# Performance work log

Measured on AMD Instinct MI355X. Metric: run time of the kernel, lower is better.

Reference implementation:

```python
import jax, jax.numpy as jnp
import numpy as np
from jax import lax

B, IMG, P, CIN = 8, 224, 16, 3
D, NH, E, HID, DEPTH, NC = 768, 12, 4, 3072, 12, 1000
NPAT = (IMG // P) ** 2  # 196
S = NPAT + 1            # 197 tokens incl cls
HD = D // NH            # 64
EPS = 1e-5


def _ln(x, g, b):
    m = jnp.mean(x, axis=-1, keepdims=True)
    v = jnp.mean((x - m) ** 2, axis=-1, keepdims=True)
    return (x - m) * lax.rsqrt(v + EPS) * g + b


def setup_inputs() -> dict:
    key = jax.random.key(0)
    ks = list(jax.random.split(key, 24))
    def rn(k, shape, s=0.02):
        return (jax.random.normal(k, shape) * s).astype(jnp.float32)
    inp = {
        "x": jax.random.normal(ks[0], (B, CIN, IMG, IMG), dtype=jnp.float32),
        "patch_w": rn(ks[1], (D, CIN, P, P)),
        "patch_b": jnp.zeros((D,), jnp.float32),
        "cls_token": jnp.zeros((1, 1, D), jnp.float32),
        "pos_embed": rn(ks[2], (1, S, D)),
        "ln1_g": jnp.ones((DEPTH, D), jnp.float32),
        "ln1_b": jnp.zeros((DEPTH, D), jnp.float32),
        "ln2_g": jnp.ones((DEPTH, D), jnp.float32),
        "ln2_b": jnp.zeros((DEPTH, D), jnp.float32),
        "attn_in_w": rn(ks[3], (DEPTH, 3 * D, D)),
        "attn_in_b": jnp.zeros((DEPTH, 3 * D), jnp.float32),
        "attn_out_w": rn(ks[4], (DEPTH, D, D)),
        "attn_out_b": jnp.zeros((DEPTH, D), jnp.float32),
        "gate_w": rn(ks[5], (DEPTH, E, D)),
        "gate_b": jnp.zeros((DEPTH, E), jnp.float32),
        "w1": rn(ks[6], (DEPTH, E, D, HID)),
        "b1": jnp.zeros((DEPTH, E, HID), jnp.float32),
        "w2": rn(ks[7], (DEPTH, E, HID, D)),
        "b2": jnp.zeros((DEPTH, E, D), jnp.float32),
        "head_w": rn(ks[8], (NC, D)),
        "head_b": jnp.zeros((NC,), jnp.float32),
    }
    return inp


def _forward(x, patch_w, patch_b, cls_token, pos_embed, ln1_g, ln1_b, ln2_g, ln2_b,
             attn_in_w, attn_in_b, attn_out_w, attn_out_b, gate_w, gate_b,
             w1, b1, w2, b2, head_w, head_b):
    # Patch embedding: conv stride=patch, then flatten spatial -> tokens
    feat = lax.conv_general_dilated(x, patch_w, window_strides=(P, P), padding="VALID",
                                    dimension_numbers=("NCHW", "OIHW", "NCHW"))
    t = feat.reshape(B, D, NPAT).transpose(0, 2, 1) + patch_b  # [B, 196, D]
    cls = jnp.broadcast_to(cls_token, (B, 1, D))
    h = jnp.concatenate([cls, t], axis=1) + pos_embed  # [B, S, D]

    scale = 1.0 / np.sqrt(HD).astype(np.float32)
    for i in range(DEPTH):
        # ---- attention (query = LN(x); key/value = x, as in source) ----
        qn = _ln(h, ln1_g[i], ln1_b[i])
        wq, wk, wv = attn_in_w[i, :D], attn_in_w[i, D:2 * D], attn_in_w[i, 2 * D:]
        bq, bk, bv = attn_in_b[i, :D], attn_in_b[i, D:2 * D], attn_in_b[i, 2 * D:]
        q = (qn @ wq.T + bq).reshape(B, S, NH, HD)
        k = (h @ wk.T + bk).reshape(B, S, NH, HD)
        v = (h @ wv.T + bv).reshape(B, S, NH, HD)
        scores = jnp.einsum("bqhd,bkhd->bhqk", q, k) * scale
        attn = jax.nn.softmax(scores, axis=-1)
        o = jnp.einsum("bhqk,bkhd->bqhd", attn, v).reshape(B, S, D)
        h = h + o @ attn_out_w[i].T + attn_out_b[i]

        # ---- Top-1 gated MoE MLP ----
        y = _ln(h, ln2_g[i], ln2_b[i])
        logits = y @ gate_w[i].T + gate_b[i]            # [B,S,E]
        probs = jax.nn.softmax(logits, axis=-1)
        top = jnp.argmax(probs, axis=-1)                # [B,S]
        onehot = jax.nn.one_hot(top, E, dtype=y.dtype)  # [B,S,E]
        gv = jnp.sum(probs * onehot, axis=-1)           # [B,S] top-1 gate score
        hidd = jax.nn.gelu(jnp.einsum("bsd,edh->besh", y, w1[i]) + b1[i][None, :, None, :])
        eout = jnp.einsum("besh,ehd->besd", hidd, w2[i]) + b2[i][None, :, None, :]
        moe = jnp.einsum("bse,besd->bsd", onehot, eout) * gv[..., None]
        h = h + moe

    return h[:, 0] @ head_w.T + head_b  # [B, NC]


def reference(x, patch_w, patch_b, cls_token, pos_embed, ln1_g, ln1_b, ln2_g, ln2_b,
              attn_in_w, attn_in_b, attn_out_w, attn_out_b, gate_w, gate_b,
              w1, b1, w2, b2, head_w, head_b):
    return _forward(x, patch_w, patch_b, cls_token, pos_embed, ln1_g, ln1_b, ln2_g,
                    ln2_b, attn_in_w, attn_in_b, attn_out_w, attn_out_b, gate_w,
                    gate_b, w1, b1, w2, b2, head_w, head_b)
```

## Files before the change

### kernel.cpp

```cpp
#include <hip/hip_runtime.h>
#include <math.h>


#define BB 8
#define SS 197
#define DD 768
#define MT (BB*SS)
#define NPATCH 196
#define MPE (BB*NPATCH)
#define HHID 3072
#define NEXP 4
#define QKVN 2304
#define SCW 228

typedef __bf16 bf16_t;
typedef bf16_t bf16x4 __attribute__((ext_vector_type(4)));
typedef bf16_t bf16x8 __attribute__((ext_vector_type(8)));
typedef float  f32x4  __attribute__((ext_vector_type(4)));

__device__ __forceinline__ void gload16(const bf16_t* g, bf16_t* l) {
    __builtin_amdgcn_global_load_lds(
        (const __attribute__((address_space(1))) unsigned int*)g,
        (__attribute__((address_space(3))) unsigned int*)l,
        16, 0, 0);
}

__device__ __forceinline__ bf16x8 cvt8(float4 a, float4 b) {
    bf16x8 o;
    o[0]=(bf16_t)a.x; o[1]=(bf16_t)a.y; o[2]=(bf16_t)a.z; o[3]=(bf16_t)a.w;
    o[4]=(bf16_t)b.x; o[5]=(bf16_t)b.y; o[6]=(bf16_t)b.z; o[7]=(bf16_t)b.w;
    return o;
}

__global__ void gather_patches(const float* __restrict__ x, bf16_t* __restrict__ Xp) {
    int i = blockIdx.x * 256 + threadIdx.x;
    if (i >= MPE * DD) return;
    int k = i % DD;
    int m = i / DD;
    int pw = k & 15, ph = (k >> 4) & 15, cin = k >> 8;
    int px = m % 14, py = (m / 14) % 14, b = m / NPATCH;
    int row = py * 16 + ph, col = px * 16 + pw;
    Xp[i] = (bf16_t)x[((size_t)(b * 3 + cin) * 224 + row) * 224 + col];
}

__global__ void build_h(const float* __restrict__ pe, const float* __restrict__ patch_b,
                        const float* __restrict__ cls, const float* __restrict__ pos,
                        float* __restrict__ h, bf16_t* __restrict__ hb) {
    int i = blockIdx.x * 256 + threadIdx.x;
    if (i >= MT * DD) return;
    int d = i % DD;
    int s = (i / DD) % SS;
    int b = i / (DD * SS);
    float v;
    if (s == 0) v = cls[d];
    else        v = pe[((size_t)(b * NPATCH) + (s - 1)) * DD + d] + patch_b[d];
    float vv = v + pos[s * DD + d];
    h[i] = vv;
    hb[i] = (bf16_t)vv;
}

__global__ void cvt_bf16(const float* __restrict__ in, bf16_t* __restrict__ out, int n) {
    int i = (blockIdx.x * 256 + threadIdx.x) * 8;
    if (i >= n) return;
    const float4* p = (const float4*)(in + i);
    *(bf16x8*)(out + i) = cvt8(p[0], p[1]);
}

__global__ __launch_bounds__(256) void transpose_cvt(const float* __restrict__ in,
                                                     bf16_t* __restrict__ out, int R, int C) {
    int z = blockIdx.z;
    in  += (size_t)z * R * C;
    out += (size_t)z * R * C;
    __shared__ float t[32][33];
    int c0 = blockIdx.x * 32, r0 = blockIdx.y * 32;
    int tx = threadIdx.x & 31, ty = threadIdx.x >> 5;
    #pragma unroll
    for (int i = 0; i < 4; i++)
        t[ty + 8*i][tx] = in[(size_t)(r0 + ty + 8*i) * C + c0 + tx];
    __syncthreads();
    #pragma unroll
    for (int i = 0; i < 4; i++)
        out[(size_t)(c0 + ty + 8*i) * R + r0 + tx] = (bf16_t)t[tx][ty + 8*i];
}

template<int BM, int BN, int WM, int WN, int MODE>
__global__ __launch_bounds__((BM/WM)*(BN/WN)*64) void gemm_bf16(
    const bf16_t* __restrict__ A, const bf16_t* __restrict__ A2, int nsplit,
    const bf16_t* __restrict__ Bw,
    const float* __restrict__ bias, float* __restrict__ C, bf16_t* __restrict__ Cb,
    const int* __restrict__ cnt, const int* __restrict__ idx,
    const float* __restrict__ gv, int M, int N, int K)
{
    constexpr int NW  = (BM/WM)*(BN/WN);
    constexpr int WNC = BN/WN;
    constexpr int MI  = WM/16;
    constexpr int NI  = WN/16;
    constexpr int IA  = (BM/8)/NW;
    constexpr int IB  = (BN/8)/NW;
    constexpr bool GATHER = (MODE == 3 || MODE == 4);

    int z = blockIdx.z;
    int count = GATHER ? cnt[z] : M;
    int m0 = blockIdx.y * BM;
    if (m0 >= count) return;
    int n0 = blockIdx.x * BN;
    if (n0 >= nsplit) A = A2;
    Bw += (size_t)z * N * K;
    const float* biasz = bias ? (bias + (size_t)z * N) : nullptr;

    __shared__ bf16_t As[2][BM * 64];
    __shared__ bf16_t Bs[2][BN * 64];
    __shared__ int toks[BM];

    int tid = threadIdx.x, lane = tid & 63, w = tid >> 6;
    if (tid < BM) {
        int mm = m0 + tid;
        if (mm > count - 1) mm = count - 1;
        toks[tid] = GATHER ? idx[z * MT + mm] : mm;
    }
    __syncthreads();

    int wm = (w / WNC) * WM, wn = (w % WNC) * WN;
    int fr = lane & 15, fs = lane >> 4;

    f32x4 acc[MI][NI];
    #pragma unroll
    for (int mi = 0; mi < MI; mi++)
        #pragma unroll
        for (int ni = 0; ni < NI; ni++)
            #pragma unroll
            for (int j = 0; j < 4; j++) acc[mi][ni][j] = 0.f;

    int nk = K >> 6;
    int srow = lane >> 3, scc = lane & 7;

    #define STAGE(buf, k0)                                                              \
        {                                                                               \
            _Pragma("unroll")                                                           \
            for (int i = 0; i < IA; i++) {                                              \
                int blk = i*NW + w;                                                     \
                int row = blk*8 + srow;                                                 \
                const bf16_t* s = A + (size_t)toks[row] * K + (k0) + ((scc ^ (row & 7)) << 3); \
                gload16(s, &As[buf][blk * 512]);                                        \
            }                                                                           \
            _Pragma("unroll")                                                           \
            for (int i = 0; i < IB; i++) {                                              \
                int blk = i*NW + w;                                                     \
                int row = blk*8 + srow;                                                 \
                const bf16_t* s = Bw + (size_t)(n0 + row) * K + (k0) + ((scc ^ (row & 7)) << 3); \
                gload16(s, &Bs[buf][blk * 512]);                                        \
            }                                                                           \
        }

    STAGE(0, 0);
    __syncthreads();
    int cur = 0;
    for (int t = 0; t < nk; t++) {
        if (t + 1 < nk) STAGE(cur ^ 1, (t + 1) << 6);
        #pragma unroll
        for (int ks = 0; ks < 2; ks++) {
            bf16x8 af[MI], bfr[NI];
            #pragma unroll
            for (int mi = 0; mi < MI; mi++) {
                int r = wm + mi * 16 + fr;
                af[mi] = *(bf16x8*)&As[cur][r * 64 + (((fs + ks*4) ^ (r & 7)) << 3)];
            }
            #pragma unroll
            for (int ni = 0; ni < NI; ni++) {
                int r = wn + ni * 16 + fr;
                bfr[ni] = *(bf16x8*)&Bs[cur][r * 64 + (((fs + ks*4) ^ (r & 7)) << 3)];
            }
            #pragma unroll
            for (int mi = 0; mi < MI; mi++)
                #pragma unroll
                for (int ni = 0; ni < NI; ni++)
                    acc[mi][ni] = __builtin_amdgcn_mfma_f32_16x16x32_bf16(af[mi], bfr[ni], acc[mi][ni], 0, 0, 0);
        }
        __syncthreads();
        cur ^= 1;
    }
    #undef STAGE

    #pragma unroll
    for (int mi = 0; mi < MI; mi++) {
        #pragma unroll
        for (int j = 0; j < 4; j++) {
            int rr = wm + mi * 16 + fs * 4 + j;
            if (m0 + rr >= count) continue;
            int crow = toks[rr];
            #pragma unroll
            for (int ni = 0; ni < NI; ni++) {
                int col = n0 + wn + ni * 16 + fr;
                float v = acc[mi][ni][j];
                if (MODE >= 2) v += biasz[col];
                if (MODE == 0) C[(size_t)crow * N + col] = v;
                else if (MODE == 2) C[(size_t)crow * N + col] += v;
                else if (MODE == 3) {
                    float g = 0.5f * v * (1.0f + tanhf(0.7978845608028654f * (v + 0.044715f * v * v * v)));
                    Cb[(size_t)crow * N + col] = (bf16_t)g;
                } else if (MODE == 4) {
                    float* p = &C[(size_t)crow * N + col];
                    float nv = *p + v * gv[crow];
                    *p = nv;
                    Cb[(size_t)crow * N + col] = (bf16_t)nv;
                } else {
                    Cb[(size_t)crow * N + col] = (bf16_t)v;
                }
            }
        }
    }
}

__global__ __launch_bounds__(256) void ln1_kernel(const float* __restrict__ x,
                                                  const float* __restrict__ g,
                                                  const float* __restrict__ b,
                                                  bf16_t* __restrict__ qn)
{
    int wid = (blockIdx.x * 256 + threadIdx.x) >> 6;
    if (wid >= MT) return;
    int lane = threadIdx.x & 63;
    const float4* xr = (const float4*)(x + (size_t)wid * DD);
    float4 v0 = xr[lane], v1 = xr[lane + 64], v2 = xr[lane + 128];
    float s = v0.x+v0.y+v0.z+v0.w + v1.x+v1.y+v1.z+v1.w + v2.x+v2.y+v2.z+v2.w;
    #pragma unroll
    for (int o = 32; o > 0; o >>= 1) s += __shfl_xor(s, o);
    float mean = s * (1.0f/DD);
    float s2 = 0.f;
    #pragma unroll
    for (int c = 0; c < 3; c++) {
        float4 v = c == 0 ? v0 : (c == 1 ? v1 : v2);
        float dx = v.x-mean, dy = v.y-mean, dz = v.z-mean, dw = v.w-mean;
        s2 += dx*dx + dy*dy + dz*dz + dw*dw;
    }
    #pragma unroll
    for (int o = 32; o > 0; o >>= 1) s2 += __shfl_xor(s2, o);
    float rs = rsqrtf(s2 * (1.0f/DD) + 1e-5f);
    const float4* gr = (const float4*)g;
    const float4* br = (const float4*)b;
    #pragma unroll
    for (int c = 0; c < 3; c++) {
        float4 v = c == 0 ? v0 : (c == 1 ? v1 : v2);
        float4 gg = gr[lane + 64*c], bb = br[lane + 64*c];
        bf16x4 o;
        o[0] = (bf16_t)((v.x - mean) * rs * gg.x + bb.x);
        o[1] = (bf16_t)((v.y - mean) * rs * gg.y + bb.y);
        o[2] = (bf16_t)((v.z - mean) * rs * gg.z + bb.z);
        o[3] = (bf16_t)((v.w - mean) * rs * gg.w + bb.w);
        *(bf16x4*)(qn + (size_t)wid * DD + (lane + 64*c) * 4) = o;
    }
}

__global__ __launch_bounds__(256) void ln2_gate_kernel(const float* __restrict__ x,
                                                       const float* __restrict__ g,
                                                       const float* __restrict__ b,
                                                       const float* __restrict__ gw,
                                                       const float* __restrict__ gb,
                                                       bf16_t* __restrict__ yb,
                                                       float* __restrict__ gv,
                                                       int* __restrict__ cnt,
                                                       int* __restrict__ idxb)
{
    int wid = (blockIdx.x * 256 + threadIdx.x) >> 6;
    if (wid >= MT) return;
    int lane = threadIdx.x & 63;
    const float4* xr = (const float4*)(x + (size_t)wid * DD);
    float4 v0 = xr[lane], v1 = xr[lane + 64], v2 = xr[lane + 128];
    float s = v0.x+v0.y+v0.z+v0.w + v1.x+v1.y+v1.z+v1.w + v2.x+v2.y+v2.z+v2.w;
    #pragma unroll
    for (int o = 32; o > 0; o >>= 1) s += __shfl_xor(s, o);
    float mean = s * (1.0f/DD);
    float s2 = 0.f;
    #pragma unroll
    for (int c = 0; c < 3; c++) {
        float4 v = c == 0 ? v0 : (c == 1 ? v1 : v2);
        float dx = v.x-mean, dy = v.y-mean, dz = v.z-mean, dw = v.w-mean;
        s2 += dx*dx + dy*dy + dz*dz + dw*dw;
    }
    #pragma unroll
    for (int o = 32; o > 0; o >>= 1) s2 += __shfl_xor(s2, o);
    float rs = rsqrtf(s2 * (1.0f/DD) + 1e-5f);
    const float4* gr = (const float4*)g;
    const float4* br = (const float4*)b;
    float p0 = 0.f, p1 = 0.f, p2 = 0.f, p3 = 0.f;
    #pragma unroll
    for (int c = 0; c < 3; c++) {
        float4 v = c == 0 ? v0 : (c == 1 ? v1 : v2);
        float4 gg = gr[lane + 64*c], bb = br[lane + 64*c];
        float y0 = (v.x - mean) * rs * gg.x + bb.x;
        float y1 = (v.y - mean) * rs * gg.y + bb.y;
        float y2 = (v.z - mean) * rs * gg.z + bb.z;
        float y3 = (v.w - mean) * rs * gg.w + bb.w;
        bf16x4 o; o[0]=(bf16_t)y0; o[1]=(bf16_t)y1; o[2]=(bf16_t)y2; o[3]=(bf16_t)y3;
        *(bf16x4*)(yb + (size_t)wid * DD + (lane + 64*c) * 4) = o;
        int off = lane + 64*c;
        float4 w0 = ((const float4*)(gw          ))[off];
        float4 w1v = ((const float4*)(gw +   DD  ))[off];
        float4 w2v = ((const float4*)(gw + 2*DD  ))[off];
        float4 w3v = ((const float4*)(gw + 3*DD  ))[off];
        p0 += y0*w0.x + y1*w0.y + y2*w0.z + y3*w0.w;
        p1 += y0*w1v.x + y1*w1v.y + y2*w1v.z + y3*w1v.w;
        p2 += y0*w2v.x + y1*w2v.y + y2*w2v.z + y3*w2v.w;
        p3 += y0*w3v.x + y1*w3v.y + y2*w3v.z + y3*w3v.w;
    }
    #pragma unroll
    for (int o = 32; o > 0; o >>= 1) {
        p0 += __shfl_xor(p0, o); p1 += __shfl_xor(p1, o);
        p2 += __shfl_xor(p2, o); p3 += __shfl_xor(p3, o);
    }
    if (lane == 0) {
        float l0 = p0 + gb[0], l1 = p1 + gb[1], l2 = p2 + gb[2], l3 = p3 + gb[3];
        int top = 0; float best = l0;
        if (l1 > best) { best = l1; top = 1; }
        if (l2 > best) { best = l2; top = 2; }
        if (l3 > best) { best = l3; top = 3; }
        float Z = __expf(l0-best) + __expf(l1-best) + __expf(l2-best) + __expf(l3-best);
        gv[wid] = 1.0f / Z;
        int pos = atomicAdd(&cnt[top], 1);
        idxb[top * MT + pos] = wid;
    }
}

__global__ __launch_bounds__(256) void attn_kernel(const bf16_t* __restrict__ qkv,
                                                   bf16_t* __restrict__ ob)
{
    int qt = blockIdx.x, hh = blockIdx.y, b = blockIdx.z;
    __shared__ bf16_t Qs[64 * 64];
    __shared__ bf16_t KV[64 * 68];
    __shared__ float  Sc[64 * SCW];
    __shared__ float  linv[64];

    int tid = threadIdx.x, lane = tid & 63, w = tid >> 6;
    int wm = (w >> 1) * 32, wn = (w & 1) * 32;
    int fr = lane & 15, fs = lane >> 4;

    #pragma unroll
    for (int it = 0; it < 2; it++) {
        int row = 8*(it*4 + w) + (lane >> 3), cc = lane & 7;
        int q = qt*64 + row; if (q > SS-1) q = SS-1;
        const bf16_t* src = qkv + ((size_t)(b*SS + q))*QKVN + hh*64 + ((cc ^ (row & 7)) << 3);
        gload16(src, &Qs[(it*4 + w) * 512]);
    }

    for (int kt = 0; kt < 4; kt++) {
        __syncthreads();
        #pragma unroll
        for (int it = 0; it < 2; it++) {
            int row = 8*(it*4 + w) + (lane >> 3), cc = lane & 7;
            int k = kt*64 + row; if (k > SS-1) k = SS-1;
            const bf16_t* src = qkv + ((size_t)(b*SS + k))*QKVN + 768 + hh*64 + ((cc ^ (row & 7)) << 3);
            gload16(src, &KV[(it*4 + w) * 512]);
        }
        __syncthreads();
        f32x4 acc[2][2];
        #pragma unroll
        for (int mi = 0; mi < 2; mi++)
            #pragma unroll
            for (int ni = 0; ni < 2; ni++)
                #pragma unroll
                for (int j = 0; j < 4; j++) acc[mi][ni][j] = 0.f;
        #pragma unroll
        for (int ks = 0; ks < 2; ks++) {
            bf16x8 af[2], bfr[2];
            #pragma unroll
            for (int mi = 0; mi < 2; mi++) {
                int r = wm + mi * 16 + fr;
                af[mi] = *(bf16x8*)&Qs[r * 64 + (((fs + ks*4) ^ (r & 7)) << 3)];
            }
            #pragma unroll
            for (int ni = 0; ni < 2; ni++) {
                int r = wn + ni * 16 + fr;
                bfr[ni] = *(bf16x8*)&KV[r * 64 + (((fs + ks*4) ^ (r & 7)) << 3)];
            }
            #pragma unroll
            for (int mi = 0; mi < 2; mi++)
                #pragma unroll
                for (int ni = 0; ni < 2; ni++)
                    acc[mi][ni] = __builtin_amdgcn_mfma_f32_16x16x32_bf16(af[mi], bfr[ni], acc[mi][ni], 0, 0, 0);
        }
        #pragma unroll
        for (int mi = 0; mi < 2; mi++)
            #pragma unroll
            for (int j = 0; j < 4; j++) {
                int qr = wm + mi * 16 + fs * 4 + j;
                #pragma unroll
                for (int ni = 0; ni < 2; ni++) {
                    int col = kt*64 + wn + ni * 16 + fr;
                    if (col < SCW) {
                        float v = acc[mi][ni][j] * 0.125f;
                        if (col > SS-1) v = -1e30f;
                        Sc[qr * SCW + col] = v;
                    }
                }
            }
    }
    __syncthreads();

    {
        int row = tid >> 2, c = tid & 3;
        float m = -1e30f;
        for (int i = c; i < SCW; i += 4) m = fmaxf(m, Sc[row * SCW + i]);
        m = fmaxf(m, __shfl_xor(m, 1, 4));
        m = fmaxf(m, __shfl_xor(m, 2, 4));
        float s = 0.f;
        for (int i = c; i < SCW; i += 4) {
            float e = __expf(Sc[row * SCW + i] - m);
            Sc[row * SCW + i] = e;
            s += e;
        }
        s += __shfl_xor(s, 1, 4);
        s += __shfl_xor(s, 2, 4);
        if (c == 0) linv[row] = 1.0f / s;
    }

    f32x4 pv[2][2];
    #pragma unroll
    for (int mi = 0; mi < 2; mi++)
        #pragma unroll
        for (int ni = 0; ni < 2; ni++)
            #pragma unroll
            for (int j = 0; j < 4; j++) pv[mi][ni][j] = 0.f;

    for (int kt = 0; kt < 4; kt++) {
        __syncthreads();
        {
            int s = tid >> 2, c2 = tid & 3;
            int k = kt*64 + s; if (k > SS-1) k = SS-1;
            const bf16_t* vr = qkv + ((size_t)(b*SS + k))*QKVN + 1536 + hh*64;
            bf16x8 v0 = *(const bf16x8*)(vr + c2*16);
            bf16x8 v1 = *(const bf16x8*)(vr + c2*16 + 8);
            #pragma unroll
            for (int j = 0; j < 8; j++) {
                KV[(c2*16 + j) * 68 + s]     = v0[j];
                KV[(c2*16 + 8 + j) * 68 + s] = v1[j];
            }
        }
        __syncthreads();
        #pragma unroll
        for (int ks = 0; ks < 2; ks++) {
            int s0 = kt*64 + ks*32;
            if (s0 > SS-1) continue;
            bf16x8 af[2], bfr[2];
            #pragma unroll
            for (int mi = 0; mi < 2; mi++) {
                int qr = wm + mi * 16 + fr;
                const float* p = &Sc[qr * SCW + s0 + fs * 8];
                af[mi] = cvt8(*(const float4*)p, *(const float4*)(p + 4));
            }
            #pragma unroll
            for (int ni = 0; ni < 2; ni++) {
                int d = wn + ni * 16 + fr;
                bfr[ni] = *(bf16x8*)&KV[d * 68 + ks*32 + fs*8];
            }
            #pragma unroll
            for (int mi = 0; mi < 2; mi++)
                #pragma unroll
                for (int ni = 0; ni < 2; ni++)
                    pv[mi][ni] = __builtin_amdgcn_mfma_f32_16x16x32_bf16(af[mi], bfr[ni], pv[mi][ni], 0, 0, 0);
        }
    }

    #pragma unroll
    for (int mi = 0; mi < 2; mi++)
        #pragma unroll
        for (int j = 0; j < 4; j++) {
            int qr = wm + mi * 16 + fs * 4 + j;
            int q = qt*64 + qr;
            if (q > SS-1) continue;
            float il = linv[qr];
            #pragma unroll
            for (int ni = 0; ni < 2; ni++) {
                int d = wn + ni * 16 + fr;
                ob[((size_t)(b*SS + q))*DD + hh*64 + d] = (bf16_t)(pv[mi][ni][j] * il);
            }
        }
}

__global__ void zero_cnt48(int* cnt) { if (threadIdx.x < 12*NEXP) cnt[threadIdx.x] = 0; }

__global__ void head_kernel(const float* __restrict__ h, const float* __restrict__ hw,
                            const float* __restrict__ hb, float* __restrict__ out)
{
    int i = blockIdx.x * 256 + threadIdx.x;
    if (i >= BB * 1000) return;
    int b = i & 7, n = i >> 3;
    const float4* hr = (const float4*)(h + (size_t)(b * SS) * DD);
    const float4* wr = (const float4*)(hw + (size_t)n * DD);
    float s = 0.f;
    #pragma unroll 4
    for (int k = 0; k < DD/4; k++) {
        float4 a = hr[k], wv = wr[k];
        s += a.x*wv.x + a.y*wv.y + a.z*wv.z + a.w*wv.w;
    }
    out[b * 1000 + n] = s + hb[n];
}

extern "C" void kernel_launch(void* const* d_in, const int* in_sizes, int n_in,
                              void* d_out, int out_size, void* d_ws, size_t ws_size,
                              hipStream_t stream) {
    const float* x          = (const float*)d_in[0];
    const float* patch_w    = (const float*)d_in[1];
    const float* patch_b    = (const float*)d_in[2];
    const float* cls_token  = (const float*)d_in[3];
    const float* pos_embed  = (const float*)d_in[4];
    const float* ln1_g      = (const float*)d_in[5];
    const float* ln1_b      = (const float*)d_in[6];
    const float* ln2_g      = (const float*)d_in[7];
    const float* ln2_b      = (const float*)d_in[8];
    const float* attn_in_w  = (const float*)d_in[9];
    const float* attn_in_b  = (const float*)d_in[10];
    const float* attn_out_w = (const float*)d_in[11];
    const float* attn_out_b = (const float*)d_in[12];
    const float* gate_w     = (const float*)d_in[13];
    const float* gate_b     = (const float*)d_in[14];
    const float* w1         = (const float*)d_in[15];
    const float* b1         = (const float*)d_in[16];
    const float* w2         = (const float*)d_in[17];
    const float* b2         = (const float*)d_in[18];
    const float* head_w     = (const float*)d_in[19];
    const float* head_b     = (const float*)d_in[20];
    float* out = (float*)d_out;

    char* wsb = (char*)d_ws;
    auto alloc = [&](size_t bytes) { char* p = wsb; wsb += (bytes + 63) & ~63ULL; return p; };
    bf16_t* Xp     = (bf16_t*)alloc((size_t)MPE * DD * 2);
    float*  pe     = (float*) alloc((size_t)MPE * DD * 4);
    float*  h      = (float*) alloc((size_t)MT * DD * 4);
    bf16_t* qn_bf  = (bf16_t*)alloc((size_t)MT * DD * 2);
    bf16_t* h_bf   = (bf16_t*)alloc((size_t)MT * DD * 2);
    bf16_t* qkv_bf = (bf16_t*)alloc((size_t)MT * QKVN * 2);
    bf16_t* ob_bf  = (bf16_t*)alloc((size_t)MT * DD * 2);
    bf16_t* yb_bf  = (bf16_t*)alloc((size_t)MT * DD * 2);
    bf16_t* hd_bf  = (bf16_t*)alloc((size_t)MT * HHID * 2);
    float*  gv     = (float*) alloc((size_t)MT * 4);
    int*    cnt    = (int*)   alloc(12 * NEXP * 4);
    int*    idxb   = (int*)   alloc((size_t)12 * NEXP * MT * 4);
    bf16_t* pw_bf  = (bf16_t*)alloc((size_t)DD * DD * 2);
    bf16_t* wq_a   = (bf16_t*)alloc((size_t)12 * QKVN * DD * 2);
    bf16_t* wo_a   = (bf16_t*)alloc((size_t)12 * DD * DD * 2);
    bf16_t* w1t_a  = (bf16_t*)alloc((size_t)12 * NEXP * DD * HHID * 2);
    bf16_t* w2t_a  = (bf16_t*)alloc((size_t)12 * NEXP * DD * HHID * 2);

    dim3 blk(256);
    dim3 blk512(512);
    const int NOSPLIT = 1 << 30;

    zero_cnt48<<<1, 64, 0, stream>>>(cnt);
    cvt_bf16<<<(DD*DD/8 + 255)/256, blk, 0, stream>>>(patch_w, pw_bf, DD*DD);
    cvt_bf16<<<(12*QKVN*DD/8 + 255)/256, blk, 0, stream>>>(attn_in_w, wq_a, 12*QKVN*DD);
    cvt_bf16<<<(12*DD*DD/8 + 255)/256, blk, 0, stream>>>(attn_out_w, wo_a, 12*DD*DD);
    transpose_cvt<<<dim3(HHID/32, DD/32, 12*NEXP), blk, 0, stream>>>(w1, w1t_a, DD, HHID);
    transpose_cvt<<<dim3(DD/32, HHID/32, 12*NEXP), blk, 0, stream>>>(w2, w2t_a, HHID, DD);

    gather_patches<<<(MPE*DD + 255)/256, blk, 0, stream>>>(x, Xp);
    gemm_bf16<64,64,32,32,0><<<dim3(12, 25, 1), blk, 0, stream>>>(
        Xp, nullptr, NOSPLIT, pw_bf, nullptr, pe, nullptr, nullptr, nullptr, nullptr, MPE, DD, DD);
    build_h<<<(MT*DD + 255)/256, blk, 0, stream>>>(pe, patch_b, cls_token, pos_embed, h, h_bf);

    for (int i = 0; i < 12; i++) {
        const bf16_t* wq_bf = wq_a  + (size_t)i * QKVN * DD;
        const bf16_t* wo_bf = wo_a  + (size_t)i * DD * DD;
        const bf16_t* w1t   = w1t_a + (size_t)i * NEXP * DD * HHID;
        const bf16_t* w2t   = w2t_a + (size_t)i * NEXP * DD * HHID;
        const float* ab    = attn_in_b  + (size_t)i * QKVN;
        const float* obias = attn_out_b + (size_t)i * DD;
        const float* l1g = ln1_g + (size_t)i * DD;
        const float* l1b = ln1_b + (size_t)i * DD;
        const float* l2g = ln2_g + (size_t)i * DD;
        const float* l2b = ln2_b + (size_t)i * DD;
        const float* gw  = gate_w + (size_t)i * NEXP * DD;
        const float* gb  = gate_b + (size_t)i * NEXP;
        const float* b1l = b1 + (size_t)i * NEXP * HHID;
        const float* b2l = b2 + (size_t)i * NEXP * DD;
        int* cnt_i  = cnt  + i * NEXP;
        int* idxb_i = idxb + (size_t)i * NEXP * MT;

        ln1_kernel<<<dim3((MT*64 + 255)/256), blk, 0, stream>>>(h, l1g, l1b, qn_bf);
        gemm_bf16<128,64,64,32,5><<<dim3(QKVN/64, 13, 1), blk, 0, stream>>>(
            qn_bf, h_bf, DD, wq_bf, ab, nullptr, qkv_bf, nullptr, nullptr, nullptr, MT, QKVN, DD);
        attn_kernel<<<dim3(4, 12, BB), blk, 0, stream>>>(qkv_bf, ob_bf);
        gemm_bf16<64,64,32,32,2><<<dim3(12, 25, 1), blk, 0, stream>>>(
            ob_bf, nullptr, NOSPLIT, wo_bf, obias, h, nullptr, nullptr, nullptr, nullptr, MT, DD, DD);
        ln2_gate_kernel<<<dim3((MT*64 + 255)/256), blk, 0, stream>>>(
            h, l2g, l2b, gw, gb, yb_bf, gv, cnt_i, idxb_i);
        gemm_bf16<128,128,64,32,3><<<dim3(HHID/128, 13, NEXP), blk512, 0, stream>>>(
            yb_bf, nullptr, NOSPLIT, w1t, b1l, nullptr, hd_bf, cnt_i, idxb_i, nullptr, MT, HHID, DD);
        gemm_bf16<64,64,32,32,4><<<dim3(12, 25, NEXP), blk, 0, stream>>>(
            hd_bf, nullptr, NOSPLIT, w2t, b2l, h, h_bf, cnt_i, idxb_i, gv, MT, DD, HHID);
    }

    head_kernel<<<(BB*1000 + 255)/256, blk, 0, stream>>>(h, head_w, head_b, out);
}
```

Baseline: 2.209 ms.

## Fuse weight fp32-to-bf16 conversion into GEMM B-tile loads and patch-embed epilogue

Drops the separate pre-pass kernels that converted and transposed all fp32 weights to bf16. The GEMM now reads fp32 weights directly into registers, converts them, and writes them into LDS, reading the transposed layout for the MoE weights. The patch-embed GEMM epilogue also adds bias and positional embedding and writes h directly, which removes build_h and the pe buffer. This saves the full weight-conversion pass but doubles the bytes read per weight tile, uses strided uncoalesced reads for the transposed w1/w2 path, and moves B staging from async LDS loads to register-staged loads that add register pressure.

```diff
diff --git a/kernel.cpp b/kernel.cpp
--- a/kernel.cpp
+++ b/kernel.cpp
@@ -43,60 +43,34 @@
     Xp[i] = (bf16_t)x[((size_t)(b * 3 + cin) * 224 + row) * 224 + col];
 }
 
-__global__ void build_h(const float* __restrict__ pe, const float* __restrict__ patch_b,
-                        const float* __restrict__ cls, const float* __restrict__ pos,
-                        float* __restrict__ h, bf16_t* __restrict__ hb) {
+__global__ void init_misc(const float* __restrict__ cls, const float* __restrict__ pos,
+                          float* __restrict__ h, bf16_t* __restrict__ hb, int* __restrict__ cnt) {
     int i = blockIdx.x * 256 + threadIdx.x;
-    if (i >= MT * DD) return;
-    int d = i % DD;
-    int s = (i / DD) % SS;
-    int b = i / (DD * SS);
-    float v;
-    if (s == 0) v = cls[d];
-    else        v = pe[((size_t)(b * NPATCH) + (s - 1)) * DD + d] + patch_b[d];
-    float vv = v + pos[s * DD + d];
-    h[i] = vv;
-    hb[i] = (bf16_t)vv;
-}
-
-__global__ void cvt_bf16(const float* __restrict__ in, bf16_t* __restrict__ out, int n) {
-    int i = (blockIdx.x * 256 + threadIdx.x) * 8;
-    if (i >= n) return;
-    const float4* p = (const float4*)(in + i);
-    *(bf16x8*)(out + i) = cvt8(p[0], p[1]);
-}
-
-__global__ __launch_bounds__(256) void transpose_cvt(const float* __restrict__ in,
-                                                     bf16_t* __restrict__ out, int R, int C) {
-    int z = blockIdx.z;
-    in  += (size_t)z * R * C;
-    out += (size_t)z * R * C;
-    __shared__ float t[32][33];
-    int c0 = blockIdx.x * 32, r0 = blockIdx.y * 32;
-    int tx = threadIdx.x & 31, ty = threadIdx.x >> 5;
-    #pragma unroll
-    for (int i = 0; i < 4; i++)
-        t[ty + 8*i][tx] = in[(size_t)(r0 + ty + 8*i) * C + c0 + tx];
-    __syncthreads();
-    #pragma unroll
-    for (int i = 0; i < 4; i++)
-        out[(size_t)(c0 + ty + 8*i) * R + r0 + tx] = (bf16_t)t[tx][ty + 8*i];
-}
-
-template<int BM, int BN, int WM, int WN, int MODE>
+    if (i < 12*NEXP) cnt[i] = 0;
+    if (i < BB * DD) {
+        int b = i / DD, d = i % DD;
+        float v = cls[d] + pos[d];
+        size_t o = (size_t)(b * SS) * DD + d;
+        h[o] = v;
+        hb[o] = (bf16_t)v;
+    }
+}
+
+template<int BM, int BN, int WM, int WN, int MODE, int BL>
 __global__ __launch_bounds__((BM/WM)*(BN/WN)*64) void gemm_bf16(
     const bf16_t* __restrict__ A, const bf16_t* __restrict__ A2, int nsplit,
-    const bf16_t* __restrict__ Bw,
+    const float* __restrict__ Bw,
     const float* __restrict__ bias, float* __restrict__ C, bf16_t* __restrict__ Cb,
     const int* __restrict__ cnt, const int* __restrict__ idx,
     const float* __restrict__ gv, int M, int N, int K)
 {
     constexpr int NW  = (BM/WM)*(BN/WN);
+    constexpr int NTH = NW * 64;
     constexpr int WNC = BN/WN;
     constexpr int MI  = WM/16;
     constexpr int NI  = WN/16;
     constexpr int IA  = (BM/8)/NW;
-    constexpr int IB  = (BN/8)/NW;
+    constexpr int BT  = (BN*8)/NTH;
     constexpr bool GATHER = (MODE == 3 || MODE == 4);
 
     int z = blockIdx.z;
@@ -134,7 +108,10 @@
     int nk = K >> 6;
     int srow = lane >> 3, scc = lane & 7;
 
-    #define STAGE(buf, k0)                                                              \
+    float4 bA[BT], bB[BT];
+    float  bt[BT][8];
+
+    #define A_STAGE(buf, k0)                                                            \
         {                                                                               \
             _Pragma("unroll")                                                           \
             for (int i = 0; i < IA; i++) {                                              \
@@ -143,20 +120,53 @@
                 const bf16_t* s = A + (size_t)toks[row] * K + (k0) + ((scc ^ (row & 7)) << 3); \
                 gload16(s, &As[buf][blk * 512]);                                        \
             }                                                                           \
+        }
+
+    #define B_LOAD(k0)                                                                  \
+        {                                                                               \
             _Pragma("unroll")                                                           \
-            for (int i = 0; i < IB; i++) {                                              \
-                int blk = i*NW + w;                                                     \
-                int row = blk*8 + srow;                                                 \
-                const bf16_t* s = Bw + (size_t)(n0 + row) * K + (k0) + ((scc ^ (row & 7)) << 3); \
-                gload16(s, &Bs[buf][blk * 512]);                                        \
+            for (int i = 0; i < BT; i++) {                                              \
+                int task = i*NTH + tid;                                                 \
+                if (BL == 0) {                                                          \
+                    int row = task >> 3, sl = task & 7;                                 \
+                    const float* s = Bw + (size_t)(n0 + row) * K + (k0) + sl*8;         \
+                    bA[i] = *(const float4*)s;                                          \
+                    bB[i] = *(const float4*)(s + 4);                                    \
+                } else {                                                                \
+                    int n = task & (BN-1), sl = task / BN;                              \
+                    const float* s = Bw + (size_t)((k0) + sl*8) * N + n0 + n;           \
+                    _Pragma("unroll")                                                   \
+                    for (int j = 0; j < 8; j++) bt[i][j] = s[(size_t)j * N];            \
+                }                                                                       \
             }                                                                           \
         }
 
-    STAGE(0, 0);
+    #define B_WRITE(buf)                                                                \
+        {                                                                               \
+            _Pragma("unroll")                                                           \
+            for (int i = 0; i < BT; i++) {                                              \
+                int task = i*NTH + tid;                                                 \
+                int row, sl;                                                            \
+                bf16x8 o;                                                               \
+                if (BL == 0) {                                                          \
+                    row = task >> 3; sl = task & 7;                                     \
+                    o = cvt8(bA[i], bB[i]);                                             \
+                } else {                                                                \
+                    row = task & (BN-1); sl = task / BN;                                \
+                    _Pragma("unroll")                                                   \
+                    for (int j = 0; j < 8; j++) o[j] = (bf16_t)bt[i][j];                \
+                }                                                                       \
+                *(bf16x8*)&Bs[buf][row * 64 + ((sl ^ (row & 7)) << 3)] = o;             \
+            }                                                                           \
+        }
+
+    A_STAGE(0, 0);
+    B_LOAD(0);
+    B_WRITE(0);
     __syncthreads();
     int cur = 0;
     for (int t = 0; t < nk; t++) {
-        if (t + 1 < nk) STAGE(cur ^ 1, (t + 1) << 6);
+        if (t + 1 < nk) { A_STAGE(cur ^ 1, (t + 1) << 6); B_LOAD((t + 1) << 6); }
         #pragma unroll
         for (int ks = 0; ks < 2; ks++) {
             bf16x8 af[MI], bfr[NI];
@@ -176,10 +186,13 @@
                 for (int ni = 0; ni < NI; ni++)
                     acc[mi][ni] = __builtin_amdgcn_mfma_f32_16x16x32_bf16(af[mi], bfr[ni], acc[mi][ni], 0, 0, 0);
         }
+        if (t + 1 < nk) B_WRITE(cur ^ 1);
         __syncthreads();
         cur ^= 1;
     }
-    #undef STAGE
+    #undef A_STAGE
+    #undef B_LOAD
+    #undef B_WRITE
 
     #pragma unroll
     for (int mi = 0; mi < MI; mi++) {
@@ -193,9 +206,9 @@
                 int col = n0 + wn + ni * 16 + fr;
                 float v = acc[mi][ni][j];
                 if (MODE >= 2) v += biasz[col];
-                if (MODE == 0) C[(size_t)crow * N + col] = v;
-                else if (MODE == 2) C[(size_t)crow * N + col] += v;
-                else if (MODE == 3) {
+                if (MODE == 2) {
+                    C[(size_t)crow * N + col] += v;
+                } else if (MODE == 3) {
                     float g = 0.5f * v * (1.0f + tanhf(0.7978845608028654f * (v + 0.044715f * v * v * v)));
                     Cb[(size_t)crow * N + col] = (bf16_t)g;
                 } else if (MODE == 4) {
@@ -203,8 +216,14 @@
                     float nv = *p + v * gv[crow];
                     *p = nv;
                     Cb[(size_t)crow * N + col] = (bf16_t)nv;
-                } else {
+                } else if (MODE == 5) {
                     Cb[(size_t)crow * N + col] = (bf16_t)v;
+                } else if (MODE == 7) {
+                    int bb = crow / NPATCH, p = crow - bb * NPATCH;
+                    size_t o = ((size_t)(bb * SS + 1 + p)) * DD + col;
+                    float vv = v + gv[(size_t)(1 + p) * DD + col];
+                    C[o] = vv;
+                    Cb[o] = (bf16_t)vv;
                 }
             }
         }
@@ -474,8 +493,6 @@
             }
         }
 }
-
-__global__ void zero_cnt48(int* cnt) { if (threadIdx.x < 12*NEXP) cnt[threadIdx.x] = 0; }
 
 __global__ void head_kernel(const float* __restrict__ h, const float* __restrict__ hw,
                             const float* __restrict__ hb, float* __restrict__ out)
@@ -523,7 +540,6 @@
     char* wsb = (char*)d_ws;
     auto alloc = [&](size_t bytes) { char* p = wsb; wsb += (bytes + 63) & ~63ULL; return p; };
     bf16_t* Xp     = (bf16_t*)alloc((size_t)MPE * DD * 2);
-    float*  pe     = (float*) alloc((size_t)MPE * DD * 4);
     float*  h      = (float*) alloc((size_t)MT * DD * 4);
     bf16_t* qn_bf  = (bf16_t*)alloc((size_t)MT * DD * 2);
     bf16_t* h_bf   = (bf16_t*)alloc((size_t)MT * DD * 2);
@@ -534,33 +550,21 @@
     float*  gv     = (float*) alloc((size_t)MT * 4);
     int*    cnt    = (int*)   alloc(12 * NEXP * 4);
     int*    idxb   = (int*)   alloc((size_t)12 * NEXP * MT * 4);
-    bf16_t* pw_bf  = (bf16_t*)alloc((size_t)DD * DD * 2);
-    bf16_t* wq_a   = (bf16_t*)alloc((size_t)12 * QKVN * DD * 2);
-    bf16_t* wo_a   = (bf16_t*)alloc((size_t)12 * DD * DD * 2);
-    bf16_t* w1t_a  = (bf16_t*)alloc((size_t)12 * NEXP * DD * HHID * 2);
-    bf16_t* w2t_a  = (bf16_t*)alloc((size_t)12 * NEXP * DD * HHID * 2);
 
     dim3 blk(256);
     dim3 blk512(512);
     const int NOSPLIT = 1 << 30;
 
-    zero_cnt48<<<1, 64, 0, stream>>>(cnt);
-    cvt_bf16<<<(DD*DD/8 + 255)/256, blk, 0, stream>>>(patch_w, pw_bf, DD*DD);
-    cvt_bf16<<<(12*QKVN*DD/8 + 255)/256, blk, 0, stream>>>(attn_in_w, wq_a, 12*QKVN*DD);
-    cvt_bf16<<<(12*DD*DD/8 + 255)/256, blk, 0, stream>>>(attn_out_w, wo_a, 12*DD*DD);
-    transpose_cvt<<<dim3(HHID/32, DD/32, 12*NEXP), blk, 0, stream>>>(w1, w1t_a, DD, HHID);
-    transpose_cvt<<<dim3(DD/32, HHID/32, 12*NEXP), blk, 0, stream>>>(w2, w2t_a, HHID, DD);
-
+    init_misc<<<24, blk, 0, stream>>>(cls_token, pos_embed, h, h_bf, cnt);
     gather_patches<<<(MPE*DD + 255)/256, blk, 0, stream>>>(x, Xp);
-    gemm_bf16<64,64,32,32,0><<<dim3(12, 25, 1), blk, 0, stream>>>(
-        Xp, nullptr, NOSPLIT, pw_bf, nullptr, pe, nullptr, nullptr, nullptr, nullptr, MPE, DD, DD);
-    build_h<<<(MT*DD + 255)/256, blk, 0, stream>>>(pe, patch_b, cls_token, pos_embed, h, h_bf);
+    gemm_bf16<64,64,32,32,7,0><<<dim3(12, 25, 1), blk, 0, stream>>>(
+        Xp, nullptr, NOSPLIT, patch_w, patch_b, h, h_bf, nullptr, nullptr, pos_embed, MPE, DD, DD);
 
     for (int i = 0; i < 12; i++) {
-        const bf16_t* wq_bf = wq_a  + (size_t)i * QKVN * DD;
-        const bf16_t* wo_bf = wo_a  + (size_t)i * DD * DD;
-        const bf16_t* w1t   = w1t_a + (size_t)i * NEXP * DD * HHID;
-        const bf16_t* w2t   = w2t_a + (size_t)i * NEXP * DD * HHID;
+        const float* aw    = attn_in_w  + (size_t)i * QKVN * DD;
+        const float* ow    = attn_out_w + (size_t)i * DD * DD;
+        const float* w1l   = w1 + (size_t)i * NEXP * DD * HHID;
+        const float* w2l   = w2 + (size_t)i * NEXP * HHID * DD;
         const float* ab    = attn_in_b  + (size_t)i * QKVN;
         const float* obias = attn_out_b + (size_t)i * DD;
         const float* l1g = ln1_g + (size_t)i * DD;
@@ -575,17 +579,17 @@
         int* idxb_i = idxb + (size_t)i * NEXP * MT;
 
         ln1_kernel<<<dim3((MT*64 + 255)/256), blk, 0, stream>>>(h, l1g, l1b, qn_bf);
-        gemm_bf16<128,64,64,32,5><<<dim3(QKVN/64, 13, 1), blk, 0, stream>>>(
-            qn_bf, h_bf, DD, wq_bf, ab, nullptr, qkv_bf, nullptr, nullptr, nullptr, MT, QKVN, DD);
+        gemm_bf16<128,64,64,32,5,0><<<dim3(QKVN/64, 13, 1), blk, 0, stream>>>(
+            qn_bf, h_bf, DD, aw, ab, nullptr, qkv_bf, nullptr, nullptr, nullptr, MT, QKVN, DD);
         attn_kernel<<<dim3(4, 12, BB), blk, 0, stream>>>(qkv_bf, ob_bf);
-        gemm_bf16<64,64,32,32,2><<<dim3(12, 25, 1), blk, 0, stream>>>(
-            ob_bf, nullptr, NOSPLIT, wo_bf, obias, h, nullptr, nullptr, nullptr, nullptr, MT, DD, DD);
+        gemm_bf16<64,64,32,32,2,0><<<dim3(12, 25, 1), blk, 0, stream>>>(
+            ob_bf, nullptr, NOSPLIT, ow, obias, h, nullptr, nullptr, nullptr, nullptr, MT, DD, DD);
         ln2_gate_kernel<<<dim3((MT*64 + 255)/256), blk, 0, stream>>>(
             h, l2g, l2b, gw, gb, yb_bf, gv, cnt_i, idxb_i);
-        gemm_bf16<128,128,64,32,3><<<dim3(HHID/128, 13, NEXP), blk512, 0, stream>>>(
-            yb_bf, nullptr, NOSPLIT, w1t, b1l, nullptr, hd_bf, cnt_i, idxb_i, nullptr, MT, HHID, DD);
-        gemm_bf16<64,64,32,32,4><<<dim3(12, 25, NEXP), blk, 0, stream>>>(
-            hd_bf, nullptr, NOSPLIT, w2t, b2l, h, h_bf, cnt_i, idxb_i, gv, MT, DD, HHID);
+        gemm_bf16<128,128,64,32,3,1><<<dim3(HHID/128, 13, NEXP), blk512, 0, stream>>>(
+            yb_bf, nullptr, NOSPLIT, w1l, b1l, nullptr, hd_bf, cnt_i, idxb_i, nullptr, MT, HHID, DD);
+        gemm_bf16<64,64,32,32,4,1><<<dim3(12, 25, NEXP), blk, 0, stream>>>(
+            hd_bf, nullptr, NOSPLIT, w2l, b2l, h, h_bf, cnt_i, idxb_i, gv, MT, DD, HHID);
     }
 
     head_kernel<<<(BB*1000 + 255)/256, blk, 0, stream>>>(h, head_w, head_b, out);
```

Result: faster. 2.139 ms (median of 2 runs) (-3.1%).
